# Performance work log

Hardware: AMD Instinct MI355X
Metric: run time of the kernel (lower is better)

## Reference

```python
import jax, jax.numpy as jnp
import numpy as np

HEADS = 8
DIM_HEAD = 64
DIM = 512
KERNEL = 33
SCALE = DIM_HEAD ** -0.5


def setup_inputs() -> dict:
    key = jax.random.key(0)
    k1, k2, k3, k4, k5, k6 = jax.random.split(key, 6)
    b, n = 2, 2048
    inner = HEADS * DIM_HEAD
    x = jax.random.normal(k1, (b, n, DIM), dtype=jnp.float32)
    mask = jax.random.uniform(k2, (b, n)) < 0.9
    W_qkv = jax.random.normal(k3, (DIM, inner * 3), dtype=jnp.float32) / np.sqrt(DIM)
    W_out = jax.random.normal(k4, (inner, DIM), dtype=jnp.float32) / np.sqrt(inner)
    b_out = jax.random.normal(k5, (DIM,), dtype=jnp.float32) * 0.01
    # depthwise Conv2d(heads, heads, (K,1), groups=heads) weight: (O=heads, I/groups=1, K, 1)
    conv_w = jax.random.normal(k6, (HEADS, 1, KERNEL, 1), dtype=jnp.float32) / np.sqrt(KERNEL)
    return {"x": x, "mask": mask, "W_qkv": W_qkv, "W_out": W_out,
            "b_out": b_out, "conv_w": conv_w}


def reference(x, mask, W_qkv, W_out, b_out, conv_w):
    b, n, _ = x.shape
    h, d = HEADS, DIM_HEAD
    qkv = (x @ W_qkv).reshape(b, n, 3, h, d)          # chunk(3) then (h d) split
    q = qkv[:, :, 0].transpose(0, 2, 1, 3)            # b h n d
    k = qkv[:, :, 1].transpose(0, 2, 1, 3)
    v = qkv[:, :, 2].transpose(0, 2, 1, 3)
    dots = jnp.einsum('bhid,bhjd->bhij', q, k) * SCALE
    mask_value = -jnp.finfo(dots.dtype).max
    dots = jnp.where(mask[:, None, None, :], dots, mask_value)
    attn = jax.nn.softmax(dots, axis=-1)
    out = jnp.einsum('bhij,bhjd->bhid', attn, v)      # b h n d
    # depthwise residual conv over sequence axis (height), per head
    pad = KERNEL // 2
    res = jax.lax.conv_general_dilated(
        v, conv_w, window_strides=(1, 1), padding=((pad, pad), (0, 0)),
        dimension_numbers=('NCHW', 'OIHW', 'NCHW'), feature_group_count=h)
    out = out + res
    out = out.transpose(0, 2, 1, 3).reshape(b, n, h * d)  # b n (h d)
    out = out @ W_out + b_out
    out = jnp.where(mask[:, :, None], out, 0.0)
    return out
```

## Files before the change

### kernel.cpp

```cpp
#include <hip/hip_runtime.h>
#include <float.h>

#define BATCH 2
#define SEQ   2048
#define HEADS 8
#define DHEAD 64
#define DIMM  512
#define NQKV  1536
#define QSCALE_L2 (0.125f * 1.44269504f)

#define QKV_ELEMS ((size_t)BATCH * HEADS * SEQ * DHEAD)
#define BHS (BATCH * HEADS * SEQ)
#define NSPLIT 4

typedef __bf16 bf16x8 __attribute__((ext_vector_type(8)));
typedef short  s16x4  __attribute__((ext_vector_type(4)));
typedef float  f32x4  __attribute__((ext_vector_type(4)));

#if __has_builtin(__builtin_amdgcn_exp2f)
#define EXP2F __builtin_amdgcn_exp2f
#else
#define EXP2F exp2f
#endif

__device__ __forceinline__ unsigned short bfbits(float f) {
  __bf16 h = (__bf16)f;
  return *(unsigned short*)&h;
}
__device__ __forceinline__ float bf2f(unsigned short u) {
  return __uint_as_float((unsigned)u << 16);
}
__device__ __forceinline__ unsigned cvtpk(float a, float b) {
  unsigned r;
  asm("v_cvt_pk_bf16_f32 %0, %1, %2" : "=v"(r) : "v"(a), "v"(b));
  return r;
}
__device__ __forceinline__ f32x4 mfma16(s16x4 a, s16x4 b, f32x4 c) {
#if __has_builtin(__builtin_amdgcn_mfma_f32_16x16x16bf16_1k)
  return __builtin_amdgcn_mfma_f32_16x16x16bf16_1k(a, b, c, 0, 0, 0);
#else
  f32x4 d;
  asm("v_mfma_f32_16x16x16_bf16 %0, %1, %2, %3" : "=v"(d) : "v"(a), "v"(b), "v"(c));
  return d;
#endif
}

__device__ __forceinline__ void transpose_tile_dev(
    const float* __restrict__ W, unsigned short* __restrict__ Wt,
    int K, int N, int n0, int k0, int t, float T[64][65]) {
  {
    int r0 = t >> 4, c4 = t & 15;
#pragma unroll
    for (int rr = 0; rr < 4; ++rr) {
      int r = r0 + rr * 16;
      float4 v = *(const float4*)(W + (size_t)(k0 + r) * N + n0 + c4 * 4);
      T[r][c4 * 4 + 0] = v.x; T[r][c4 * 4 + 1] = v.y;
      T[r][c4 * 4 + 2] = v.z; T[r][c4 * 4 + 3] = v.w;
    }
  }
  __syncthreads();
  {
    int n = t >> 2, kc = t & 3;
    union { unsigned short u[16]; int4 v[2]; } p;
#pragma unroll
    for (int i = 0; i < 16; ++i) p.u[i] = bfbits(T[kc * 16 + i][n]);
    int4* dst = (int4*)(Wt + (size_t)(n0 + n) * K + k0 + kc * 16);
    dst[0] = p.v[0]; dst[1] = p.v[1];
  }
}

__global__ __launch_bounds__(256) void prep_all(
    const float* __restrict__ X, const void* __restrict__ mraw,
    const float* __restrict__ Wqkv, const float* __restrict__ Wout,
    unsigned short* __restrict__ Xbf, float* __restrict__ maskf,
    unsigned short* __restrict__ Wtq, unsigned short* __restrict__ Wto,
    unsigned* __restrict__ kmaxn) {
  __shared__ float T[64][65];
  __shared__ int f_bf16, f_f32, f_gt1, f_oddnz;
  const int b = blockIdx.x;
  const int t = threadIdx.x;
  if (b < 1024) {
    size_t i = ((size_t)b * 256 + t) * 8;
    float4 a0 = *(const float4*)(X + i);
    float4 a1 = *(const float4*)(X + i + 4);
    union { unsigned short u[8]; int4 v; } pk;
    pk.u[0] = bfbits(a0.x); pk.u[1] = bfbits(a0.y);
    pk.u[2] = bfbits(a0.z); pk.u[3] = bfbits(a0.w);
    pk.u[4] = bfbits(a1.x); pk.u[5] = bfbits(a1.y);
    pk.u[6] = bfbits(a1.z); pk.u[7] = bfbits(a1.w);
    *(int4*)(Xbf + i) = pk.v;
  } else if (b < 1216) {
    int bb2 = b - 1024;
    transpose_tile_dev(Wqkv, Wtq, DIMM, NQKV, (bb2 % 24) * 64, (bb2 / 24) * 64, t, T);
  } else if (b < 1280) {
    int bb2 = b - 1216;
    transpose_tile_dev(Wout, Wto, DIMM, DIMM, (bb2 & 7) * 64, (bb2 >> 3) * 64, t, T);
  } else {
    if (t < 16) kmaxn[t] = 0u;
    if (t == 0) { f_bf16 = 0; f_f32 = 0; f_gt1 = 0; f_oddnz = 0; }
    __syncthreads();
    const unsigned int* w = (const unsigned int*)mraw;
    unsigned int v = w[t];
    if (v == 0x3f803f80u) f_bf16 = 1;
    if (v == 0x3f800000u) f_f32 = 1;
    if (v > 1u)           f_gt1 = 1;
    if ((t & 1) && v != 0u) f_oddnz = 1;
    __syncthreads();
    int mode;
    if (f_bf16)       mode = 4;
    else if (f_f32)   mode = 3;
    else if (f_gt1)   mode = 1;
    else if (!f_oddnz) mode = 2;
    else              mode = 0;
    for (int i = t; i < BATCH * SEQ; i += 256) {
      bool keep;
      if (mode == 4)      keep = ((const unsigned short*)mraw)[i] != 0;
      else if (mode == 3) keep = ((const float*)mraw)[i] != 0.f;
      else if (mode == 1) keep = ((const unsigned char*)mraw)[i] != 0;
      else if (mode == 2) keep = w[2 * i] != 0u;
      else                keep = w[i] != 0u;
      maskf[i] = keep ? 1.f : 0.f;
    }
  }
}

__global__ __launch_bounds__(256) void gemm_qkv_mfma(
    const unsigned short* __restrict__ Xbf, const unsigned short* __restrict__ Wt,
    unsigned short* __restrict__ Qbf, unsigned short* __restrict__ Kbf,
    unsigned short* __restrict__ Vt, unsigned* __restrict__ kmaxn) {
  __shared__ __align__(16) unsigned char Al[128 * 128];
  __shared__ __align__(16) unsigned char Bl[64 * 128];
  const int tid = threadIdx.x;
  const int lane = tid & 63;
  const int w = tid >> 6;
  const int l15 = lane & 15, g = lane >> 4;
  const int wr = w >> 1, wc = w & 1;
  int bid = blockIdx.x;
  int lid = (bid & 7) * 96 + (bid >> 3);
  int by = lid / 24, bx = lid - by * 24;
  const int m0 = by * 128;

  f32x4 acc[4][2] = {};
  const int srow = tid >> 3, scg = tid & 7;
  const int rsw = (l15 & 7) << 4;

  for (int k0 = 0; k0 < DIMM; k0 += 64) {
    __syncthreads();
#pragma unroll
    for (int it = 0; it < 4; ++it) {
      int row = srow + it * 32;
      int sw = (row & 7) << 4;
      *(int4*)(Al + row * 128 + ((scg * 16) ^ sw)) =
          *(const int4*)(Xbf + (size_t)(m0 + row) * DIMM + k0 + scg * 8);
      if (it < 2) {
        *(int4*)(Bl + row * 128 + ((scg * 16) ^ sw)) =
            *(const int4*)(Wt + (size_t)(bx * 64 + row) * DIMM + k0 + scg * 8);
      }
    }
    __syncthreads();
#pragma unroll
    for (int ks = 0; ks < 2; ++ks) {
      bf16x8 af[4], bfr[2];
#pragma unroll
      for (int mi = 0; mi < 4; ++mi)
        af[mi] = *(const bf16x8*)(Al + (wr * 64 + mi * 16 + l15) * 128 +
                                  ((ks * 64 + g * 16) ^ rsw));
#pragma unroll
      for (int nj = 0; nj < 2; ++nj)
        bfr[nj] = *(const bf16x8*)(Bl + (wc * 32 + nj * 16 + l15) * 128 +
                                   ((ks * 64 + g * 16) ^ rsw));
#pragma unroll
      for (int mi = 0; mi < 4; ++mi)
#pragma unroll
        for (int nj = 0; nj < 2; ++nj)
          acc[mi][nj] = __builtin_amdgcn_mfma_f32_16x16x32_bf16(
              af[mi], bfr[nj], acc[mi][nj], 0, 0, 0);
    }
  }
  const int chunk = bx >> 3;
  const int bb = m0 >> 11;
#pragma unroll
  for (int nj = 0; nj < 2; ++nj) {
    int col = (bx & 7) * 64 + wc * 32 + nj * 16 + l15;
    int hh = col >> 6, dd = col & 63;
#pragma unroll
    for (int mi = 0; mi < 4; ++mi) {
      int ii0 = (m0 & (SEQ - 1)) + wr * 64 + mi * 16 + g * 4;
      if (chunk == 2) {
        union { unsigned short u[4]; ushort4 v; } pk;
#pragma unroll
        for (int r = 0; r < 4; ++r) pk.u[r] = bfbits(acc[mi][nj][r]);
        *(ushort4*)(Vt + ((size_t)(bb * HEADS + hh) * DHEAD + dd) * SEQ + ii0) = pk.v;
      } else {
        unsigned short* dst = (chunk == 0) ? Qbf : Kbf;
        float sc = (chunk == 0) ? QSCALE_L2 : 1.f;
#pragma unroll
        for (int r = 0; r < 4; ++r)
          dst[((size_t)(bb * HEADS + hh) * SEQ + ii0 + r) * DHEAD + dd] =
              bfbits(acc[mi][nj][r] * sc);
      }
    }
  }
  if (chunk == 1) {
    float kab = 0.f;
#pragma unroll
    for (int nj = 0; nj < 2; ++nj)
#pragma unroll
      for (int mi = 0; mi < 4; ++mi)
#pragma unroll
        for (int r = 0; r < 4; ++r) kab = fmaxf(kab, fabsf(acc[mi][nj][r]));
#pragma unroll
    for (int d = 1; d < 64; d <<= 1) kab = fmaxf(kab, __shfl_xor(kab, d));
    if (lane == 0)
      atomicMax(kmaxn + (bb * HEADS + (bx & 7)), __float_as_uint(kab * 1.005f));
  }
}

__global__ __launch_bounds__(256) void attn_split(const unsigned short* __restrict__ Qbf,
                                                  const unsigned short* __restrict__ Kbf,
                                                  const unsigned short* __restrict__ Vt,
                                                  const float* __restrict__ maskf,
                                                  const unsigned* __restrict__ kmaxn,
                                                  unsigned short* __restrict__ Po,
                                                  float* __restrict__ LSE) {
  __shared__ __align__(16) unsigned char Ks[16384];
  __shared__ __align__(16) unsigned char Vs[16384];

  const int tid = threadIdx.x;
  const int lane = tid & 63;
  const int w = tid >> 6;
  const int l15 = lane & 15, g = lane >> 4;

  int fid = blockIdx.x;
  int lid = (fid & 7) * 256 + (fid >> 3);
  const int bh = lid >> 7;
  const int rem = lid & 127;
  const int qb = rem >> 2;
  const int quarter = rem & 3;
  const int bb = bh >> 3;

  const unsigned short* Qg = Qbf + ((size_t)bh * SEQ + qb * 64) * DHEAD;
  const unsigned short* Kg = Kbf + (size_t)bh * SEQ * DHEAD;
  const unsigned short* Vg = Vt  + (size_t)bh * DHEAD * SEQ;
  const float* mrow = maskf + bb * SEQ;

  bf16x8 qf0, qf1;
  {
    const unsigned char* qrow = (const unsigned char*)(Qg + (size_t)(w * 16 + l15) * DHEAD);
    qf0 = *(const bf16x8*)(qrow + g * 16);
    qf1 = *(const bf16x8*)(qrow + 64 + g * 16);
  }
  float Bx, Bnat;
  {
    float qn2 = 0.f;
#pragma unroll
    for (int i = 0; i < 8; ++i) {
      float a = (float)qf0[i]; qn2 += a * a;
      float b = (float)qf1[i]; qn2 += b * b;
    }
    qn2 += __shfl_xor(qn2, 16);
    qn2 += __shfl_xor(qn2, 32);
    const float kabs = __uint_as_float(kmaxn[bh]);
    Bx = sqrtf(qn2) * 8.f * kabs;
    Bnat = Bx * 0.69314718f;
  }

  f32x4 o[4] = {};
  float lsum = 0.f;

  const int sm = tid >> 2;
  const int sc = (tid & 3) * 32;
  const int ssw = (sm & 7) << 4;
  const int vswap = (sm >> 3) & 1;
  const int rsw = (l15 & 7) << 4;
  const int vsw = rsw | (((l15 >> 3) & 1) << 3);
  const int kt0 = quarter * 8;

  int4 rk0, rk1, rv0, rv1;
  {
    const unsigned char* ksrc =
        (const unsigned char*)(Kg + (size_t)kt0 * 64 * DHEAD) + sm * 128 + sc;
    const unsigned char* vsrc =
        (const unsigned char*)(Vg + (size_t)sm * SEQ + kt0 * 64) + sc;
    rk0 = *(const int4*)(ksrc); rk1 = *(const int4*)(ksrc + 16);
    rv0 = *(const int4*)(vsrc); rv1 = *(const int4*)(vsrc + 16);
  }
  {
    *(int4*)(Ks + sm * 128 + ((sc)      ^ ssw)) = rk0;
    *(int4*)(Ks + sm * 128 + ((sc + 16) ^ ssw)) = rk1;
    int4 sv0 = vswap ? (int4){rv0.z, rv0.w, rv0.x, rv0.y} : rv0;
    int4 sv1 = vswap ? (int4){rv1.z, rv1.w, rv1.x, rv1.y} : rv1;
    *(int4*)(Vs + sm * 128 + ((sc)      ^ ssw)) = sv0;
    *(int4*)(Vs + sm * 128 + ((sc + 16) ^ ssw)) = sv1;
  }
  __syncthreads();

  for (int t = 0; t < 8; ++t) {
    const int kt = kt0 + t;
    const int co = (t & 1) << 13;
    const int no = co ^ 8192;
    float4 km[4];
#pragma unroll
    for (int j = 0; j < 4; ++j) km[j] = *(const float4*)(mrow + kt * 64 + 16 * j + 4 * g);
    if (t < 7) {
      const unsigned char* ksrc =
          (const unsigned char*)(Kg + (size_t)(kt + 1) * 64 * DHEAD) + sm * 128 + sc;
      const unsigned char* vsrc =
          (const unsigned char*)(Vg + (size_t)sm * SEQ + (kt + 1) * 64) + sc;
      rk0 = *(const int4*)(ksrc); rk1 = *(const int4*)(ksrc + 16);
      rv0 = *(const int4*)(vsrc); rv1 = *(const int4*)(vsrc + 16);
    }

    f32x4 s[4];
#pragma unroll
    for (int j = 0; j < 4; ++j) {
      const unsigned char* krow = Ks + co + (16 * j + l15) * 128;
      bf16x8 kf0 = *(const bf16x8*)(krow + ((g * 16)      ^ rsw));
      bf16x8 kf1 = *(const bf16x8*)(krow + ((64 + g * 16) ^ rsw));
      f32x4 z = (f32x4){0.f, 0.f, 0.f, 0.f};
      z = __builtin_amdgcn_mfma_f32_16x16x32_bf16(kf0, qf0, z, 0, 0, 0);
      z = __builtin_amdgcn_mfma_f32_16x16x32_bf16(kf1, qf1, z, 0, 0, 0);
      s[j] = z;
    }

    s16x4 pa[4];
#pragma unroll
    for (int j = 0; j < 4; ++j) {
      float p0 = EXP2F(s[j][0] - Bx) * km[j].x;
      float p1 = EXP2F(s[j][1] - Bx) * km[j].y;
      float p2 = EXP2F(s[j][2] - Bx) * km[j].z;
      float p3 = EXP2F(s[j][3] - Bx) * km[j].w;
      lsum += (p0 + p1) + (p2 + p3);
      union { uint2 u; s16x4 v; } pk;
      pk.u.x = cvtpk(p0, p1);
      pk.u.y = cvtpk(p2, p3);
      pa[j] = pk.v;
    }

#pragma unroll
    for (int dj = 0; dj < 4; ++dj) {
      const unsigned char* vrow = Vs + co + (16 * dj + l15) * 128;
#pragma unroll
      for (int j = 0; j < 4; ++j) {
        s16x4 vb = *(const s16x4*)(vrow + ((32 * j + 8 * g) ^ vsw));
        o[dj] = mfma16(pa[j], vb, o[dj]);
      }
    }

    if (t < 7) {
      *(int4*)(Ks + no + sm * 128 + ((sc)      ^ ssw)) = rk0;
      *(int4*)(Ks + no + sm * 128 + ((sc + 16) ^ ssw)) = rk1;
      int4 sv0 = vswap ? (int4){rv0.z, rv0.w, rv0.x, rv0.y} : rv0;
      int4 sv1 = vswap ? (int4){rv1.z, rv1.w, rv1.x, rv1.y} : rv1;
      *(int4*)(Vs + no + sm * 128 + ((sc)      ^ ssw)) = sv0;
      *(int4*)(Vs + no + sm * 128 + ((sc + 16) ^ ssw)) = sv1;
      __syncthreads();
    }
  }

  lsum += __shfl_xor(lsum, 16);
  lsum += __shfl_xor(lsum, 32);
#pragma unroll
  for (int r = 0; r < 4; ++r) {
    float lr = __shfl(lsum, 4 * g + r);
    float inv = (lr > 0.f) ? 1.f / lr : 0.f;
    int row = qb * 64 + w * 16 + 4 * g + r;
    size_t base = (size_t)quarter * QKV_ELEMS + ((size_t)bh * SEQ + row) * DHEAD + l15;
    Po[base]      = bfbits(o[0][r] * inv);
    Po[base + 16] = bfbits(o[1][r] * inv);
    Po[base + 32] = bfbits(o[2][r] * inv);
    Po[base + 48] = bfbits(o[3][r] * inv);
  }
  if (g == 0) {
    int row = qb * 64 + w * 16 + l15;
    LSE[quarter * BHS + bh * SEQ + row] =
        (lsum > 0.f) ? Bnat + __logf(lsum) : -3.0e38f;
  }
}

__global__ __launch_bounds__(256) void combine_conv(
    const unsigned short* __restrict__ Po, const float* __restrict__ LSE,
    const unsigned short* __restrict__ Vt, const float* __restrict__ cw,
    unsigned short* __restrict__ Obf) {
  __shared__ float T[96][68];
  __shared__ float cwl[33];
  const int tid = threadIdx.x;
  const int bid = blockIdx.x;
  const int bh = bid >> 5;
  const int n0 = (bid & 31) * 64;
  const int hh = bh & 7;
  if (tid < 33) cwl[tid] = cw[hh * 33 + tid];
  for (int idx = tid; idx < 64 * 24; idx += 256) {
    int d = idx / 24, c4 = idx - (idx / 24) * 24;
    int nbase = n0 - 16 + c4 * 4;
    const unsigned short* src = Vt + ((size_t)bh * DHEAD + d) * SEQ;
#pragma unroll
    for (int q = 0; q < 4; ++q) {
      int n = nbase + q;
      T[c4 * 4 + q][d] = (n >= 0 && n < SEQ) ? bf2f(src[n]) : 0.f;
    }
  }
  __syncthreads();
#pragma unroll
  for (int p = 0; p < 4; ++p) {
    int n = (tid >> 4) + p * 16;
    int d4 = tid & 15;
    int row = bh * SEQ + n0 + n;
    float ls[NSPLIT], m = -3.0e38f;
#pragma unroll
    for (int q = 0; q < NSPLIT; ++q) { ls[q] = LSE[q * BHS + row]; m = fmaxf(m, ls[q]); }
    float wq[NSPLIT], tot = 0.f;
#pragma unroll
    for (int q = 0; q < NSPLIT; ++q) { wq[q] = __expf(ls[q] - m); tot += wq[q]; }
    float inv = 1.f / tot;
    float o0 = 0.f, o1 = 0.f, o2 = 0.f, o3 = 0.f;
#pragma unroll
    for (int q = 0; q < NSPLIT; ++q) {
      float wk = wq[q] * inv;
      ushort4 a = *(const ushort4*)(Po + (size_t)q * QKV_ELEMS + (size_t)row * DHEAD + d4 * 4);
      o0 += wk * bf2f(a.x); o1 += wk * bf2f(a.y);
      o2 += wk * bf2f(a.z); o3 += wk * bf2f(a.w);
    }
#pragma unroll
    for (int t = 0; t < 33; ++t) {
      float wv = cwl[t];
      float4 tv = *(const float4*)&T[n + t][d4 * 4];
      o0 += wv * tv.x; o1 += wv * tv.y; o2 += wv * tv.z; o3 += wv * tv.w;
    }
    union { unsigned short u[4]; ushort4 v; } pk;
    pk.u[0] = bfbits(o0); pk.u[1] = bfbits(o1);
    pk.u[2] = bfbits(o2); pk.u[3] = bfbits(o3);
    *(ushort4*)(Obf + (size_t)row * DHEAD + d4 * 4) = pk.v;
  }
}

__global__ __launch_bounds__(256) void gemm_out_mfma(
    const unsigned short* __restrict__ Obf, const unsigned short* __restrict__ Wt,
    const float* __restrict__ bias, const float* __restrict__ maskf,
    float* __restrict__ out) {
  __shared__ __align__(16) unsigned char Al[64 * 128];
  __shared__ __align__(16) unsigned char Bl[64 * 128];
  const int tid = threadIdx.x;
  const int lane = tid & 63;
  const int w = tid >> 6;
  const int l15 = lane & 15, g = lane >> 4;
  const int wr = w >> 1, wc = w & 1;
  int bid = blockIdx.x;
  int lid = (bid & 7) * 64 + (bid >> 3);
  int by = lid >> 3, bx = lid & 7;
  const int m0 = by * 64, n0 = bx * 64;
  const int bb = m0 >> 11;
  const int ii0 = m0 & (SEQ - 1);

  f32x4 acc[2][2] = {};
  const int srow = tid >> 3, scg = tid & 7;
  const int rsw = (l15 & 7) << 4;

  for (int k0 = 0; k0 < DIMM; k0 += 64) {
    const int hh = k0 >> 6;
    __syncthreads();
#pragma unroll
    for (int it = 0; it < 2; ++it) {
      int row = srow + it * 32;
      int sw = (row & 7) << 4;
      *(int4*)(Al + row * 128 + ((scg * 16) ^ sw)) =
          *(const int4*)(Obf + ((size_t)(bb * HEADS + hh) * SEQ + ii0 + row) * DHEAD + scg * 8);
      *(int4*)(Bl + row * 128 + ((scg * 16) ^ sw)) =
          *(const int4*)(Wt + (size_t)(n0 + row) * DIMM + k0 + scg * 8);
    }
    __syncthreads();
#pragma unroll
    for (int ks = 0; ks < 2; ++ks) {
      bf16x8 af[2], bfr[2];
#pragma unroll
      for (int mi = 0; mi < 2; ++mi)
        af[mi] = *(const bf16x8*)(Al + (wr * 32 + mi * 16 + l15) * 128 +
                                  ((ks * 64 + g * 16) ^ rsw));
#pragma unroll
      for (int nj = 0; nj < 2; ++nj)
        bfr[nj] = *(const bf16x8*)(Bl + (wc * 32 + nj * 16 + l15) * 128 +
                                   ((ks * 64 + g * 16) ^ rsw));
#pragma unroll
      for (int mi = 0; mi < 2; ++mi)
#pragma unroll
        for (int nj = 0; nj < 2; ++nj)
          acc[mi][nj] = __builtin_amdgcn_mfma_f32_16x16x32_bf16(
              af[mi], bfr[nj], acc[mi][nj], 0, 0, 0);
    }
  }
#pragma unroll
  for (int nj = 0; nj < 2; ++nj) {
    int col = n0 + wc * 32 + nj * 16 + l15;
    float bcol = bias[col];
#pragma unroll
    for (int mi = 0; mi < 2; ++mi) {
#pragma unroll
      for (int r = 0; r < 4; ++r) {
        int m = m0 + wr * 32 + mi * 16 + g * 4 + r;
        out[(size_t)m * DIMM + col] = (acc[mi][nj][r] + bcol) * maskf[m];
      }
    }
  }
}

extern "C" void kernel_launch(void* const* d_in, const int* in_sizes, int n_in,
                              void* d_out, int out_size, void* d_ws, size_t ws_size,
                              hipStream_t stream) {
  const float* x     = (const float*)d_in[0];
  const void*  mask  = d_in[1];
  const float* Wqkv  = (const float*)d_in[2];
  const float* Wout  = (const float*)d_in[3];
  const float* bout  = (const float*)d_in[4];
  const float* convw = (const float*)d_in[5];
  float* out = (float*)d_out;

  float* maskf = (float*)d_ws;
  unsigned* kmaxn = (unsigned*)(maskf + 4096);
  unsigned short* Qbf = (unsigned short*)(kmaxn + 64);
  unsigned short* Kbf = Qbf + QKV_ELEMS;
  unsigned short* Vt  = Kbf + QKV_ELEMS;
  unsigned short* Po  = Vt + QKV_ELEMS;
  float* LSE          = (float*)(Po + NSPLIT * QKV_ELEMS);
  unsigned short* Obf = (unsigned short*)(LSE + NSPLIT * BHS);
  unsigned short* Wtq = Obf + QKV_ELEMS;
  unsigned short* Wto = Wtq + (size_t)NQKV * DIMM;
  unsigned short* Xbf = Wto + (size_t)DIMM * DIMM;

  prep_all<<<1281, 256, 0, stream>>>(x, mask, Wqkv, Wout, Xbf, maskf, Wtq, Wto, kmaxn);
  gemm_qkv_mfma<<<768, 256, 0, stream>>>(Xbf, Wtq, Qbf, Kbf, Vt, kmaxn);
  attn_split<<<2048, 256, 0, stream>>>(Qbf, Kbf, Vt, maskf, kmaxn, Po, LSE);
  combine_conv<<<512, 256, 0, stream>>>(Po, LSE, Vt, convw, Obf);
  gemm_out_mfma<<<512, 256, 0, stream>>>(Obf, Wto, bout, maskf, out);
}
```

Baseline: 99.55 us.

## Stage Q/K epilogue through LDS for coalesced stores; combine splits via raw sums

The QKV GEMM epilogue for Q and K now writes the bf16 tile into shared memory with a swizzle and then emits 16-byte coalesced row stores, replacing the scattered 2-byte global stores. Separately, the split attention stops normalizing each partial output and computing a log-sum-exp. It stores unnormalized partial outputs and raw row sums instead, so the combine kernel can simply sum them and divide once. This works because every split shares the same fixed bound offset. The cost is extra LDS traffic and syncs in the epilogue, and unnormalized partials stored in bf16 may lose some precision.

```diff
diff --git a/kernel.cpp b/kernel.cpp
--- a/kernel.cpp
+++ b/kernel.cpp
@@ -179,40 +179,60 @@
   }
   const int chunk = bx >> 3;
   const int bb = m0 >> 11;
-#pragma unroll
-  for (int nj = 0; nj < 2; ++nj) {
-    int col = (bx & 7) * 64 + wc * 32 + nj * 16 + l15;
-    int hh = col >> 6, dd = col & 63;
-#pragma unroll
-    for (int mi = 0; mi < 4; ++mi) {
-      int ii0 = (m0 & (SEQ - 1)) + wr * 64 + mi * 16 + g * 4;
-      if (chunk == 2) {
+  const int hh = bx & 7;
+  if (chunk == 2) {
+#pragma unroll
+    for (int nj = 0; nj < 2; ++nj) {
+      int dd = wc * 32 + nj * 16 + l15;
+#pragma unroll
+      for (int mi = 0; mi < 4; ++mi) {
+        int ii0 = (m0 & (SEQ - 1)) + wr * 64 + mi * 16 + g * 4;
         union { unsigned short u[4]; ushort4 v; } pk;
 #pragma unroll
         for (int r = 0; r < 4; ++r) pk.u[r] = bfbits(acc[mi][nj][r]);
         *(ushort4*)(Vt + ((size_t)(bb * HEADS + hh) * DHEAD + dd) * SEQ + ii0) = pk.v;
-      } else {
-        unsigned short* dst = (chunk == 0) ? Qbf : Kbf;
-        float sc = (chunk == 0) ? QSCALE_L2 : 1.f;
-#pragma unroll
-        for (int r = 0; r < 4; ++r)
-          dst[((size_t)(bb * HEADS + hh) * SEQ + ii0 + r) * DHEAD + dd] =
+      }
+    }
+  } else {
+    if (chunk == 1) {
+      float kab = 0.f;
+#pragma unroll
+      for (int nj = 0; nj < 2; ++nj)
+#pragma unroll
+        for (int mi = 0; mi < 4; ++mi)
+#pragma unroll
+          for (int r = 0; r < 4; ++r) kab = fmaxf(kab, fabsf(acc[mi][nj][r]));
+#pragma unroll
+      for (int d = 1; d < 64; d <<= 1) kab = fmaxf(kab, __shfl_xor(kab, d));
+      if (lane == 0)
+        atomicMax(kmaxn + (bb * HEADS + hh), __float_as_uint(kab * 1.005f));
+    }
+    unsigned short* dst = (chunk == 0) ? Qbf : Kbf;
+    const float sc = (chunk == 0) ? QSCALE_L2 : 1.f;
+    __syncthreads();
+#pragma unroll
+    for (int nj = 0; nj < 2; ++nj) {
+      int dd = wc * 32 + nj * 16 + l15;
+#pragma unroll
+      for (int mi = 0; mi < 4; ++mi) {
+#pragma unroll
+        for (int r = 0; r < 4; ++r) {
+          int rowl = wr * 64 + mi * 16 + g * 4 + r;
+          *(unsigned short*)(Al + rowl * 128 + ((dd * 2) ^ ((rowl & 7) << 4))) =
               bfbits(acc[mi][nj][r] * sc);
+        }
       }
     }
-  }
-  if (chunk == 1) {
-    float kab = 0.f;
-#pragma unroll
-    for (int nj = 0; nj < 2; ++nj)
-#pragma unroll
-      for (int mi = 0; mi < 4; ++mi)
-#pragma unroll
-        for (int r = 0; r < 4; ++r) kab = fmaxf(kab, fabsf(acc[mi][nj][r]));
-#pragma unroll
-    for (int d = 1; d < 64; d <<= 1) kab = fmaxf(kab, __shfl_xor(kab, d));
-    if (lane == 0)
-      atomicMax(kmaxn + (bb * HEADS + (bx & 7)), __float_as_uint(kab * 1.005f));
+    __syncthreads();
+    const int rr = tid >> 1, hf = tid & 1;
+    const int ii0 = (m0 & (SEQ - 1));
+    unsigned short* gout =
+        dst + ((size_t)(bb * HEADS + hh) * SEQ + ii0 + rr) * DHEAD + hf * 32;
+    const int sw2 = (rr & 7) << 4;
+#pragma unroll
+    for (int q = 0; q < 4; ++q)
+      *(int4*)(gout + q * 8) =
+          *(const int4*)(Al + rr * 128 + ((hf * 64 + q * 16) ^ sw2));
   }
 }
 
@@ -222,7 +242,7 @@
                                                   const float* __restrict__ maskf,
                                                   const unsigned* __restrict__ kmaxn,
                                                   unsigned short* __restrict__ Po,
-                                                  float* __restrict__ LSE) {
+                                                  float* __restrict__ LSUM) {
   __shared__ __align__(16) unsigned char Ks[16384];
   __shared__ __align__(16) unsigned char Vs[16384];
 
@@ -250,7 +270,7 @@
     qf0 = *(const bf16x8*)(qrow + g * 16);
     qf1 = *(const bf16x8*)(qrow + 64 + g * 16);
   }
-  float Bx, Bnat;
+  float Bx;
   {
     float qn2 = 0.f;
 #pragma unroll
@@ -262,7 +282,6 @@
     qn2 += __shfl_xor(qn2, 32);
     const float kabs = __uint_as_float(kmaxn[bh]);
     Bx = sqrtf(qn2) * 8.f * kabs;
-    Bnat = Bx * 0.69314718f;
   }
 
   f32x4 o[4] = {};
@@ -358,28 +377,25 @@
     }
   }
 
+#pragma unroll
+  for (int r = 0; r < 4; ++r) {
+    int row = qb * 64 + w * 16 + 4 * g + r;
+    size_t base = (size_t)quarter * QKV_ELEMS + ((size_t)bh * SEQ + row) * DHEAD + l15;
+    Po[base]      = bfbits(o[0][r]);
+    Po[base + 16] = bfbits(o[1][r]);
+    Po[base + 32] = bfbits(o[2][r]);
+    Po[base + 48] = bfbits(o[3][r]);
+  }
   lsum += __shfl_xor(lsum, 16);
   lsum += __shfl_xor(lsum, 32);
-#pragma unroll
-  for (int r = 0; r < 4; ++r) {
-    float lr = __shfl(lsum, 4 * g + r);
-    float inv = (lr > 0.f) ? 1.f / lr : 0.f;
-    int row = qb * 64 + w * 16 + 4 * g + r;
-    size_t base = (size_t)quarter * QKV_ELEMS + ((size_t)bh * SEQ + row) * DHEAD + l15;
-    Po[base]      = bfbits(o[0][r] * inv);
-    Po[base + 16] = bfbits(o[1][r] * inv);
-    Po[base + 32] = bfbits(o[2][r] * inv);
-    Po[base + 48] = bfbits(o[3][r] * inv);
-  }
   if (g == 0) {
     int row = qb * 64 + w * 16 + l15;
-    LSE[quarter * BHS + bh * SEQ + row] =
-        (lsum > 0.f) ? Bnat + __logf(lsum) : -3.0e38f;
+    LSUM[quarter * BHS + bh * SEQ + row] = lsum;
   }
 }
 
 __global__ __launch_bounds__(256) void combine_conv(
-    const unsigned short* __restrict__ Po, const float* __restrict__ LSE,
+    const unsigned short* __restrict__ Po, const float* __restrict__ LSUM,
     const unsigned short* __restrict__ Vt, const float* __restrict__ cw,
     unsigned short* __restrict__ Obf) {
   __shared__ float T[96][68];
@@ -406,21 +422,18 @@
     int n = (tid >> 4) + p * 16;
     int d4 = tid & 15;
     int row = bh * SEQ + n0 + n;
-    float ls[NSPLIT], m = -3.0e38f;
-#pragma unroll
-    for (int q = 0; q < NSPLIT; ++q) { ls[q] = LSE[q * BHS + row]; m = fmaxf(m, ls[q]); }
-    float wq[NSPLIT], tot = 0.f;
-#pragma unroll
-    for (int q = 0; q < NSPLIT; ++q) { wq[q] = __expf(ls[q] - m); tot += wq[q]; }
-    float inv = 1.f / tot;
+    float tot = 0.f;
+#pragma unroll
+    for (int q = 0; q < NSPLIT; ++q) tot += LSUM[q * BHS + row];
+    float inv = (tot > 0.f) ? 1.f / tot : 0.f;
     float o0 = 0.f, o1 = 0.f, o2 = 0.f, o3 = 0.f;
 #pragma unroll
     for (int q = 0; q < NSPLIT; ++q) {
-      float wk = wq[q] * inv;
       ushort4 a = *(const ushort4*)(Po + (size_t)q * QKV_ELEMS + (size_t)row * DHEAD + d4 * 4);
-      o0 += wk * bf2f(a.x); o1 += wk * bf2f(a.y);
-      o2 += wk * bf2f(a.z); o3 += wk * bf2f(a.w);
-    }
+      o0 += bf2f(a.x); o1 += bf2f(a.y);
+      o2 += bf2f(a.z); o3 += bf2f(a.w);
+    }
+    o0 *= inv; o1 *= inv; o2 *= inv; o3 *= inv;
 #pragma unroll
     for (int t = 0; t < 33; ++t) {
       float wv = cwl[t];
@@ -520,15 +533,15 @@
   unsigned short* Kbf = Qbf + QKV_ELEMS;
   unsigned short* Vt  = Kbf + QKV_ELEMS;
   unsigned short* Po  = Vt + QKV_ELEMS;
-  float* LSE          = (float*)(Po + NSPLIT * QKV_ELEMS);
-  unsigned short* Obf = (unsigned short*)(LSE + NSPLIT * BHS);
+  float* LSUM         = (float*)(Po + NSPLIT * QKV_ELEMS);
+  unsigned short* Obf = (unsigned short*)(LSUM + NSPLIT * BHS);
   unsigned short* Wtq = Obf + QKV_ELEMS;
   unsigned short* Wto = Wtq + (size_t)NQKV * DIMM;
   unsigned short* Xbf = Wto + (size_t)DIMM * DIMM;
 
   prep_all<<<1281, 256, 0, stream>>>(x, mask, Wqkv, Wout, Xbf, maskf, Wtq, Wto, kmaxn);
   gemm_qkv_mfma<<<768, 256, 0, stream>>>(Xbf, Wtq, Qbf, Kbf, Vt, kmaxn);
-  attn_split<<<2048, 256, 0, stream>>>(Qbf, Kbf, Vt, maskf, kmaxn, Po, LSE);
-  combine_conv<<<512, 256, 0, stream>>>(Po, LSE, Vt, convw, Obf);
+  attn_split<<<2048, 256, 0, stream>>>(Qbf, Kbf, Vt, maskf, kmaxn, Po, LSUM);
+  combine_conv<<<512, 256, 0, stream>>>(Po, LSUM, Vt, convw, Obf);
   gemm_out_mfma<<<512, 256, 0, stream>>>(Obf, Wto, bout, maskf, out);
 }
```

Measured after the change: 99.00 us. Within noise of the previous version (-0.5%).
